# Performance work log

Hardware: AMD Instinct MI355X
Metric: run time of the kernel (lower is better)

The kernel has to match this reference:

```python
import jax, jax.numpy as jnp
import numpy as np

B, D_IMG, H, VOCAB, T = 16384, 2048, 512, 200, 20

def setup_inputs() -> dict:
    key = jax.random.key(0)
    ks = jax.random.split(key, 24)
    def w(k, shape, scale=0.05):
        return jax.random.normal(k, shape, dtype=jnp.float32) * scale
    return {
        "images": jax.random.normal(ks[0], (B, D_IMG), dtype=jnp.float32),
        "actions": jax.random.randint(ks[1], (B, T), 0, VOCAB, dtype=jnp.int64),
        # encoder: Linear(2048,512) -> ReLU -> Linear(512,512)
        "enc_w1": w(ks[2], (H, D_IMG)), "enc_b1": jnp.zeros((H,), jnp.float32),
        "enc_w2": w(ks[3], (H, H)),     "enc_b2": jnp.zeros((H,), jnp.float32),
        # GRUCell(512,512): gate order r, z, n (PyTorch convention)
        "gru_wih": w(ks[4], (3 * H, H)), "gru_bih": jnp.zeros((3 * H,), jnp.float32),
        "gru_whh": w(ks[5], (3 * H, H)), "gru_bhh": jnp.zeros((3 * H,), jnp.float32),
        # actor: 512->64->64->vocab
        "act_w1": w(ks[6], (64, H)),   "act_b1": jnp.zeros((64,), jnp.float32),
        "act_w2": w(ks[7], (64, 64)),  "act_b2": jnp.zeros((64,), jnp.float32),
        "act_w3": w(ks[8], (VOCAB, 64), 0.01), "act_b3": jnp.zeros((VOCAB,), jnp.float32),
        # critic: 512->64->64->1
        "cri_w1": w(ks[9], (64, H)),   "cri_b1": jnp.zeros((64,), jnp.float32),
        "cri_w2": w(ks[10], (64, 64)), "cri_b2": jnp.zeros((64,), jnp.float32),
        "cri_w3": w(ks[11], (1, 64), 0.02), "cri_b3": jnp.zeros((1,), jnp.float32),
    }

def reference(images, actions, enc_w1, enc_b1, enc_w2, enc_b2,
              gru_wih, gru_bih, gru_whh, gru_bhh,
              act_w1, act_b1, act_w2, act_b2, act_w3, act_b3,
              cri_w1, cri_b1, cri_w2, cri_b2, cri_w3, cri_b3):
    # encoder
    x = jax.nn.relu(images @ enc_w1.T + enc_b1) @ enc_w2.T + enc_b2  # [B, H]
    # input-side GRU gates are constant across steps (same x every step)
    xg = x @ gru_wih.T + gru_bih                                     # [B, 3H]
    xr, xz, xn = jnp.split(xg, 3, axis=-1)

    def step(hx, a_t):
        hg = hx @ gru_whh.T + gru_bhh
        hr, hz, hn = jnp.split(hg, 3, axis=-1)
        r = jax.nn.sigmoid(xr + hr)
        z = jax.nn.sigmoid(xz + hz)
        n = jnp.tanh(xn + r * hn)
        hx = (1.0 - z) * n + z * hx                                   # [B, H]
        # actor head -> categorical stats
        a_h = jnp.tanh(jnp.tanh(hx @ act_w1.T + act_b1) @ act_w2.T + act_b2)
        logits = a_h @ act_w3.T + act_b3                              # [B, V]
        logp = jax.nn.log_softmax(logits, axis=-1)
        lp = jnp.take_along_axis(logp, a_t[:, None], axis=1)[:, 0]    # [B]
        ent = -jnp.sum(jnp.exp(logp) * logp, axis=-1)                 # [B]
        # critic head
        c_h = jnp.tanh(jnp.tanh(hx @ cri_w1.T + cri_b1) @ cri_w2.T + cri_b2)
        v = c_h @ cri_w3.T + cri_b3                                   # [B, 1]
        return hx, (lp, ent, v)

    hx0 = jnp.zeros_like(x)
    _, (lps, ents, vs) = jax.lax.scan(step, hx0, actions.T)           # [T, B, ...]
    logprobs = lps.T                                                  # [B, T]
    entropies = ents.T                                                # [B, T]
    values = jnp.transpose(vs, (1, 0, 2))                             # [B, T, 1]
    return actions, logprobs, entropies, values
```

## Files before the change

### kernel.cpp

```cpp
#include <hip/hip_runtime.h>
#include <hip/hip_fp16.h>
#include <cstddef>
#include <cstdint>

#define BB 16384
#define DIMG 2048
#define HH 512
#define VOCAB 200
#define TT 20

using frag16 = __attribute__((ext_vector_type(8))) short;
using f32x4v = __attribute__((ext_vector_type(4))) float;

#define MFMA16(a, b, c) __builtin_amdgcn_mfma_f32_16x16x32_bf16((a), (b), (c), 0, 0, 0)

__device__ __forceinline__ float bf2f(unsigned short u) {
    union { unsigned int i; float f; } c; c.i = ((unsigned int)u) << 16; return c.f;
}
__device__ __forceinline__ unsigned short f2bf(float f) {
    union { float f; unsigned int i; } c; c.f = f;
    unsigned int u = c.i;
    u = (u + 0x7FFFu + ((u >> 16) & 1u)) >> 16;
    return (unsigned short)u;
}
__device__ __forceinline__ float sigf(float x) { return 1.f / (1.f + __expf(-x)); }
__device__ __forceinline__ float ftanh(float x) {
    return 1.f - 2.f / (1.f + __expf(2.f * x));
}
__device__ __forceinline__ void gload16(const void* g, void* l) {
    __builtin_amdgcn_global_load_lds(
        (__attribute__((address_space(1))) void*)g,
        (__attribute__((address_space(3))) void*)l, 16, 0, 0);
}


template<int ACT, int OM>
__global__ __launch_bounds__(256) void gemm_bt_mfma(
    const unsigned short* __restrict__ A, const unsigned short* __restrict__ W,
    const float* __restrict__ bias, void* __restrict__ Cv, int M, int N, int K)
{
    __shared__ unsigned short As[128 * 32];
    __shared__ unsigned short Ws[128 * 32];
    const int t = threadIdx.x;
    const int lane = t & 63, w = t >> 6;
    const int bm = blockIdx.x, bn = blockIdx.y;
    const int wm = (w >> 1) * 64, wn = (w & 1) * 64;

    f32x4v acc[4][4];
    #pragma unroll
    for (int i = 0; i < 4; ++i)
        #pragma unroll
        for (int j = 0; j < 4; ++j)
            #pragma unroll
            for (int r = 0; r < 4; ++r) acc[i][j][r] = 0.f;

    const unsigned short* Ag  = A + (size_t)(bm * 128 + (t >> 2)) * K + (t & 3) * 8;
    const unsigned short* Ag2 = A + (size_t)(bm * 128 + 64 + (t >> 2)) * K + (t & 3) * 8;
    const unsigned short* Wg  = W + (size_t)(bn * 128 + (t >> 2)) * K + (t & 3) * 8;
    const unsigned short* Wg2 = W + (size_t)(bn * 128 + 64 + (t >> 2)) * K + (t & 3) * 8;
    char* AsB = (char*)As; char* WsB = (char*)Ws;

    const int kIters = K >> 5;
    for (int ki = 0; ki < kIters; ++ki) {
        const int k0 = ki * 32;
        gload16(Ag  + k0, AsB + w * 1024);
        gload16(Ag2 + k0, AsB + 4096 + w * 1024);
        gload16(Wg  + k0, WsB + w * 1024);
        gload16(Wg2 + k0, WsB + 4096 + w * 1024);
        __syncthreads();
        frag16 af[4], bf[4];
        #pragma unroll
        for (int i = 0; i < 4; ++i) {
            af[i] = *(const frag16*)(AsB + (wm + i * 16 + (lane & 15)) * 64 + (lane >> 4) * 16);
            bf[i] = *(const frag16*)(WsB + (wn + i * 16 + (lane & 15)) * 64 + (lane >> 4) * 16);
        }
        #pragma unroll
        for (int i = 0; i < 4; ++i)
            #pragma unroll
            for (int j = 0; j < 4; ++j)
                acc[i][j] = MFMA16(af[i], bf[j], acc[i][j]);
        __syncthreads();
    }

    #pragma unroll
    for (int j = 0; j < 4; ++j) {
        const int gn = bn * 128 + wn + j * 16 + (lane & 15);
        const float bv = bias[gn];
        #pragma unroll
        for (int i = 0; i < 4; ++i) {
            #pragma unroll
            for (int r = 0; r < 4; ++r) {
                const size_t gm = (size_t)(bm * 128 + wm + i * 16 + (lane >> 4) * 4 + r);
                float v = acc[i][j][r] + bv;
                if (ACT == 1) v = fmaxf(v, 0.f);
                if (OM == 0)      ((float*)Cv)[gm * N + gn] = v;
                else if (OM == 1) ((unsigned short*)Cv)[gm * N + gn] = f2bf(v);
                else              ((__half*)Cv)[gm * N + gn] = __float2half(v);
            }
        }
    }
}

__device__ __forceinline__ void gru_body(
    unsigned short* lds,
    const unsigned short* __restrict__ hb, unsigned short* __restrict__ hob,
    const unsigned short* __restrict__ whhb, const float* __restrict__ bhh,
    const __half* __restrict__ xg, int bm, int bn, int t)
{
    char* L  = (char*)lds;
    char* LW = L + 16384;
    const int lane = t & 63, w = t >> 6;
    const int q = lane >> 4, m = lane & 15;
    const int qs = q ^ ((m >> 1) & 3);
    const int scol = ((t & 3) ^ ((t >> 3) & 3)) * 8;

    f32x4v acc[2][3][4];
    #pragma unroll
    for (int i = 0; i < 2; ++i)
        #pragma unroll
        for (int g = 0; g < 3; ++g)
            #pragma unroll
            for (int j = 0; j < 4; ++j)
                #pragma unroll
                for (int r = 0; r < 4; ++r) acc[i][g][j][r] = 0.f;

    const unsigned short* Ag  = hb + (size_t)(bm * 128 + (t >> 2)) * HH + scol;
    const unsigned short* Wg0 = whhb + (size_t)(0 * HH + bn * 64 + (t >> 2)) * HH + scol;
    const unsigned short* Wg1 = whhb + (size_t)(1 * HH + bn * 64 + (t >> 2)) * HH + scol;
    const unsigned short* Wg2 = whhb + (size_t)(2 * HH + bn * 64 + (t >> 2)) * HH + scol;

    for (int ki = 0; ki < 8; ++ki) {
        const int k0 = ki * 64;
        gload16(Ag + k0,                          L + w * 1024);
        gload16(Ag + k0 + 32,                     L + 8192 + w * 1024);
        gload16(Ag + (size_t)64 * HH + k0,        L + 4096 + w * 1024);
        gload16(Ag + (size_t)64 * HH + k0 + 32,   L + 8192 + 4096 + w * 1024);
        gload16(Wg0 + k0,      LW + w * 1024);
        gload16(Wg0 + k0 + 32, LW + 12288 + w * 1024);
        gload16(Wg1 + k0,      LW + 4096 + w * 1024);
        gload16(Wg1 + k0 + 32, LW + 12288 + 4096 + w * 1024);
        gload16(Wg2 + k0,      LW + 8192 + w * 1024);
        gload16(Wg2 + k0 + 32, LW + 12288 + 8192 + w * 1024);
        __syncthreads();
        #pragma unroll
        for (int kk = 0; kk < 2; ++kk) {
            frag16 af0 = *(const frag16*)(L + kk * 8192 +        (w * 16 + m) * 64 + qs * 16);
            frag16 af1 = *(const frag16*)(L + kk * 8192 + 4096 + (w * 16 + m) * 64 + qs * 16);
            #pragma unroll
            for (int g = 0; g < 3; ++g)
                #pragma unroll
                for (int j = 0; j < 4; ++j) {
                    frag16 bf = *(const frag16*)(LW + kk * 12288 + g * 4096 + (j * 16 + m) * 64 + qs * 16);
                    acc[0][g][j] = MFMA16(af0, bf, acc[0][g][j]);
                    acc[1][g][j] = MFMA16(af1, bf, acc[1][g][j]);
                }
        }
        __syncthreads();
    }

    float br[4], bz[4], bnn[4];
    #pragma unroll
    for (int j = 0; j < 4; ++j) {
        const int gc = bn * 64 + j * 16 + m;
        br[j] = bhh[gc]; bz[j] = bhh[HH + gc]; bnn[j] = bhh[2 * HH + gc];
    }

    #pragma unroll
    for (int half = 0; half < 2; ++half) {
        const int rbase = bm * 128 + half * 64;
        const __half* Xg = xg + (size_t)(rbase + (t >> 3)) * (3 * HH) + bn * 64 + (t & 7) * 8;
        #pragma unroll
        for (int c = 0; c < 6; ++c) {
            const int g = c >> 1, rh = c & 1;
            gload16(Xg + (size_t)rh * 32 * (3 * HH) + g * HH, L + g * 8192 + rh * 4096 + w * 1024);
        }
        const unsigned short* Hg = hb + (size_t)(rbase + (t >> 3)) * HH + bn * 64 + (t & 7) * 8;
        gload16(Hg,                   L + 24576 + w * 1024);
        gload16(Hg + (size_t)32 * HH, L + 24576 + 4096 + w * 1024);
        __syncthreads();

        unsigned short hv[4][4];
        #pragma unroll
        for (int r = 0; r < 4; ++r) {
            const int row = w * 16 + q * 4 + r;
            #pragma unroll
            for (int j = 0; j < 4; ++j) {
                const int col2 = (j * 16 + m) * 2;
                const float xr = __half2float(*(const __half*)(L + row * 128 + col2));
                const float xz = __half2float(*(const __half*)(L + 8192 + row * 128 + col2));
                const float xn = __half2float(*(const __half*)(L + 16384 + row * 128 + col2));
                const float ho = bf2f(*(const unsigned short*)(L + 24576 + row * 128 + col2));
                const float rg = sigf(xr + acc[half][0][j][r] + br[j]);
                const float zg = sigf(xz + acc[half][1][j][r] + bz[j]);
                const float ng = ftanh(xn + rg * (acc[half][2][j][r] + bnn[j]));
                hv[r][j] = f2bf((1.f - zg) * ng + zg * ho);
            }
        }
        __syncthreads();
        #pragma unroll
        for (int r = 0; r < 4; ++r) {
            const int row = w * 16 + q * 4 + r;
            #pragma unroll
            for (int j = 0; j < 4; ++j)
                *(unsigned short*)(L + 24576 + row * 128 + (j * 16 + m) * 2) = hv[r][j];
        }
        __syncthreads();
        {
            const int sr = t >> 2, sc = (t & 3) * 16;
            uint4 v0 = *(const uint4*)(L + 24576 + sr * 128 + sc * 2);
            uint4 v1 = *(const uint4*)(L + 24576 + sr * 128 + sc * 2 + 16);
            unsigned short* dst = hob + (size_t)(rbase + sr) * HH + bn * 64 + sc;
            *(uint4*)dst = v0;
            *(uint4*)(dst + 8) = v1;
        }
        __syncthreads();
    }
}

__device__ __forceinline__ void heads_body(
    unsigned short* lds, const unsigned short* __restrict__ hxb,
    const unsigned short* __restrict__ w1c, const unsigned short* __restrict__ w2s,
    const unsigned short* __restrict__ w3s,
    const float* __restrict__ b1c, const float* __restrict__ b2c,
    const float* __restrict__ b3s,
    const float* __restrict__ cw3, const float* __restrict__ cb3,
    const int* __restrict__ actions,
    float* __restrict__ out_lp, float* __restrict__ out_ent,
    float* __restrict__ out_v, int tstep, int hblk, int t)
{
    char* sH = (char*)lds;
    char* sW = (char*)lds + 4096;
    unsigned short* u1 = lds;
    const int lane = t & 63, w = t >> 6;
    const int q = lane >> 4, m = lane & 15;
    const int qs = q ^ ((m >> 1) & 3);
    const int scol = ((t & 3) ^ ((t >> 3) & 3)) * 8;
    const int row0 = hblk * 32;
    const int ri = (w & 1) * 16, ch = (w >> 1) * 64;

    f32x4v acc[4];
    #pragma unroll
    for (int j = 0; j < 4; ++j)
        #pragma unroll
        for (int r = 0; r < 4; ++r) acc[j][r] = 0.f;

    const unsigned short* Hrow = hxb + (size_t)(row0 + ((t >> 2) & 31)) * HH
                                 + (t >> 7) * 32 + scol;
    const unsigned short* Wrow[4]; int WldsOff[4];
    #pragma unroll
    for (int c = 0; c < 4; ++c) {
        const int kk = c & 1, rb = (c >> 1) * 64;
        Wrow[c] = w1c + (size_t)(rb + (t >> 2)) * HH + kk * 32 + scol;
        WldsOff[c] = kk * 8192 + rb * 64;
    }

    for (int ki = 0; ki < 8; ++ki) {
        const int k0 = ki * 64;
        gload16(Hrow + k0, sH + w * 1024);
        #pragma unroll
        for (int c = 0; c < 4; ++c)
            gload16(Wrow[c] + k0, sW + WldsOff[c] + w * 1024);
        __syncthreads();
        #pragma unroll
        for (int kk = 0; kk < 2; ++kk) {
            frag16 af = *(const frag16*)(sH + kk * 2048 + (ri + m) * 64 + qs * 16);
            #pragma unroll
            for (int j = 0; j < 4; ++j) {
                frag16 bf = *(const frag16*)(sW + kk * 8192 + (ch + j * 16 + m) * 64 + qs * 16);
                acc[j] = MFMA16(af, bf, acc[j]);
            }
        }
        __syncthreads();
    }
    #pragma unroll
    for (int j = 0; j < 4; ++j) {
        const int col = ch + j * 16 + m;
        const float bv = b1c[col];
        #pragma unroll
        for (int r = 0; r < 4; ++r)
            u1[(ri + q * 4 + r) * 136 + col] = f2bf(ftanh(acc[j][r] + bv));
    }
    __syncthreads();

    f32x4v acc2[4];
    #pragma unroll
    for (int j = 0; j < 4; ++j)
        #pragma unroll
        for (int r = 0; r < 4; ++r) acc2[j][r] = 0.f;
    #pragma unroll
    for (int kk = 0; kk < 2; ++kk) {
        frag16 af2 = *(const frag16*)(u1 + (ri + m) * 136 + ch + kk * 32 + q * 8);
        #pragma unroll
        for (int j = 0; j < 4; ++j) {
            frag16 bf2 = *(const frag16*)(w2s + (size_t)(ch + j * 16 + m) * 64 + kk * 32 + q * 8);
            acc2[j] = MFMA16(af2, bf2, acc2[j]);
        }
    }
    __syncthreads();
    #pragma unroll
    for (int j = 0; j < 4; ++j) {
        const int col = ch + j * 16 + m;
        const float bv = b2c[col];
        #pragma unroll
        for (int r = 0; r < 4; ++r)
            u1[(ri + q * 4 + r) * 136 + col] = f2bf(ftanh(acc2[j][r] + bv));
    }
    __syncthreads();

    if (w < 2) {
        f32x4v acc3[13];
        #pragma unroll
        for (int j = 0; j < 13; ++j)
            #pragma unroll
            for (int r = 0; r < 4; ++r) acc3[j][r] = 0.f;
        #pragma unroll
        for (int kk = 0; kk < 2; ++kk) {
            frag16 af3 = *(const frag16*)(u1 + (w * 16 + m) * 136 + kk * 32 + q * 8);
            #pragma unroll
            for (int j = 0; j < 13; ++j) {
                frag16 bf3 = *(const frag16*)(w3s + (size_t)(j * 16 + m) * 64 + kk * 32 + q * 8);
                acc3[j] = MFMA16(af3, bf3, acc3[j]);
            }
        }
        float bcol[13];
        #pragma unroll
        for (int j = 0; j < 13; ++j) bcol[j] = b3s[j * 16 + m];
        const bool vlast = (m < 8);
        #pragma unroll
        for (int r = 0; r < 4; ++r) {
            const int gr = row0 + w * 16 + 4 * q + r;
            const int a = actions[(size_t)gr * TT + tstep];
            float lg[13], mx = -1e30f;
            #pragma unroll
            for (int j = 0; j < 13; ++j) {
                float v = acc3[j][r] + bcol[j];
                lg[j] = (j < 12 || vlast) ? v : -1e30f;
                mx = fmaxf(mx, lg[j]);
            }
            #pragma unroll
            for (int o = 1; o < 16; o <<= 1) mx = fmaxf(mx, __shfl_xor(mx, o));
            float s1 = 0.f, s2 = 0.f, sel = 0.f;
            #pragma unroll
            for (int j = 0; j < 13; ++j) {
                float e = __expf(lg[j] - mx);
                s1 += e; s2 += e * lg[j];
                sel += (j * 16 + m == a) ? lg[j] : 0.f;
            }
            #pragma unroll
            for (int o = 1; o < 16; o <<= 1) {
                s1 += __shfl_xor(s1, o); s2 += __shfl_xor(s2, o); sel += __shfl_xor(sel, o);
            }
            const float lse = mx + __logf(s1);
            if (m == 0) {
                out_lp[(size_t)gr * TT + tstep]  = sel - lse;
                out_ent[(size_t)gr * TT + tstep] = lse - s2 / s1;
            }
        }
    } else {
        const int row = (w - 2) * 16 + m;
        const unsigned short* u2row = u1 + row * 136 + 64 + q * 16;
        float pv = 0.f;
        #pragma unroll
        for (int kk = 0; kk < 16; ++kk)
            pv += bf2f(u2row[kk]) * cw3[q * 16 + kk];
        pv += __shfl_xor(pv, 16);
        pv += __shfl_xor(pv, 32);
        if (q == 0) out_v[(size_t)(row0 + row) * TT + tstep] = pv + cb3[0];
    }
}

__global__ __launch_bounds__(256, 3) void step_fused(
    const unsigned short* __restrict__ hin, unsigned short* __restrict__ hout,
    const unsigned short* __restrict__ whhb, const float* __restrict__ bhh,
    const __half* __restrict__ xg,
    const unsigned short* __restrict__ w1c, const unsigned short* __restrict__ w2s,
    const unsigned short* __restrict__ w3s,
    const float* __restrict__ b1c, const float* __restrict__ b2c,
    const float* __restrict__ b3s,
    const float* __restrict__ cw3, const float* __restrict__ cb3,
    const int* __restrict__ actions,
    float* __restrict__ out_lp, float* __restrict__ out_ent,
    float* __restrict__ out_v, int hstep)
{
    __shared__ unsigned short lds[20480];
    const int b = blockIdx.x;
    if (b < 1024) {
        const int bm = ((b >> 6) << 3) | (b & 7);
        const int bn = (b >> 3) & 7;
        gru_body(lds, hin, hout, whhb, bhh, xg, bm, bn, threadIdx.x);
    } else if (hstep >= 0) {
        heads_body(lds, hin, w1c, w2s, w3s, b1c, b2c, b3s, cw3, cb3,
                   actions, out_lp, out_ent, out_v, hstep, b - 1024, threadIdx.x);
    }
}

__global__ __launch_bounds__(256) void heads_tail(
    const unsigned short* __restrict__ hx,
    const unsigned short* __restrict__ w1c, const unsigned short* __restrict__ w2s,
    const unsigned short* __restrict__ w3s,
    const float* __restrict__ b1c, const float* __restrict__ b2c,
    const float* __restrict__ b3s,
    const float* __restrict__ cw3, const float* __restrict__ cb3,
    const int* __restrict__ actions,
    float* __restrict__ out_lp, float* __restrict__ out_ent,
    float* __restrict__ out_v, int tstep)
{
    __shared__ unsigned short lds[10240];
    heads_body(lds, hx, w1c, w2s, w3s, b1c, b2c, b3s, cw3, cb3,
               actions, out_lp, out_ent, out_v, tstep, blockIdx.x, threadIdx.x);
}

__global__ void prep_heads(
    const float* __restrict__ aw1, const float* __restrict__ cw1,
    const float* __restrict__ aw2, const float* __restrict__ cw2,
    const float* __restrict__ aw3,
    const float* __restrict__ ab1, const float* __restrict__ cb1,
    const float* __restrict__ ab2, const float* __restrict__ cb2,
    const float* __restrict__ ab3,
    unsigned short* __restrict__ w1c, unsigned short* __restrict__ w2s,
    unsigned short* __restrict__ w3s,
    float* __restrict__ b1c, float* __restrict__ b2c, float* __restrict__ b3s)
{
    int i = blockIdx.x * 256 + threadIdx.x;
    if (i < 65536) { int r = i >> 9, c = i & 511;
        w1c[i] = f2bf(r < 64 ? aw1[r * 512 + c] : cw1[(r - 64) * 512 + c]); return; }
    i -= 65536;
    if (i < 8192) { int r = i >> 6, c = i & 63;
        w2s[i] = f2bf(r < 64 ? aw2[r * 64 + c] : cw2[(r - 64) * 64 + c]); return; }
    i -= 8192;
    if (i < 13312) { int r = i >> 6, c = i & 63;
        w3s[i] = f2bf(r < 200 ? aw3[r * 64 + c] : 0.f); return; }
    i -= 13312;
    if (i < 128) { b1c[i] = i < 64 ? ab1[i] : cb1[i - 64]; return; }
    i -= 128;
    if (i < 128) { b2c[i] = i < 64 ? ab2[i] : cb2[i - 64]; return; }
    i -= 128;
    if (i < 208) { b3s[i] = i < 200 ? ab3[i] : 0.f; return; }
}

__global__ void f2b_kernel(const float* __restrict__ s, unsigned short* __restrict__ d, int n) {
    int i = (blockIdx.x * 256 + threadIdx.x) * 4;
    if (i < n) {
        float4 v = *(const float4*)(s + i);
        ushort4 o;
        o.x = f2bf(v.x); o.y = f2bf(v.y); o.z = f2bf(v.z); o.w = f2bf(v.w);
        *(ushort4*)(d + i) = o;
    }
}

__global__ void copy_actions(const int* __restrict__ a, float* __restrict__ o, int n) {
    int i = blockIdx.x * 256 + threadIdx.x;
    if (i < n) o[i] = (float)a[i];
}

extern "C" void kernel_launch(void* const* d_in, const int* in_sizes, int n_in,
                              void* d_out, int out_size, void* d_ws, size_t ws_size,
                              hipStream_t stream)
{
    const float* images = (const float*)d_in[0];
    const int*   actions = (const int*)d_in[1];
    const float* enc_w1 = (const float*)d_in[2];
    const float* enc_b1 = (const float*)d_in[3];
    const float* enc_w2 = (const float*)d_in[4];
    const float* enc_b2 = (const float*)d_in[5];
    const float* gru_wih = (const float*)d_in[6];
    const float* gru_bih = (const float*)d_in[7];
    const float* gru_whh = (const float*)d_in[8];
    const float* gru_bhh = (const float*)d_in[9];
    const float* act_w1 = (const float*)d_in[10];
    const float* act_b1 = (const float*)d_in[11];
    const float* act_w2 = (const float*)d_in[12];
    const float* act_b2 = (const float*)d_in[13];
    const float* act_w3 = (const float*)d_in[14];
    const float* act_b3 = (const float*)d_in[15];
    const float* cri_w1 = (const float*)d_in[16];
    const float* cri_b1 = (const float*)d_in[17];
    const float* cri_w2 = (const float*)d_in[18];
    const float* cri_b2 = (const float*)d_in[19];
    const float* cri_w3 = (const float*)d_in[20];
    const float* cri_b3 = (const float*)d_in[21];

    char* ws = (char*)d_ws;
    unsigned short* imgb = (unsigned short*)ws;
    __half*         xg   = (__half*)ws;
    unsigned short* hbA  = (unsigned short*)(ws + 67108864);
    unsigned short* hbB  = (unsigned short*)(ws + 83886080);
    unsigned short* w1b  = (unsigned short*)(ws + 100663296);
    unsigned short* w2b  = (unsigned short*)(ws + 102760448);
    unsigned short* wihb = (unsigned short*)(ws + 103284736);
    unsigned short* whhb = (unsigned short*)(ws + 104857600);
    unsigned short* w1c  = (unsigned short*)(ws + 106430464);
    unsigned short* w2s  = (unsigned short*)(ws + 106561536);
    unsigned short* w3s  = (unsigned short*)(ws + 106577920);
    float*          b1c  = (float*)(ws + 106604544);
    float*          b2c  = (float*)(ws + 106605056);
    float*          b3s  = (float*)(ws + 106605568);

    float* out_act = (float*)d_out;
    float* out_lp  = out_act + (size_t)BB * TT;
    float* out_ent = out_lp  + (size_t)BB * TT;
    float* out_v   = out_ent + (size_t)BB * TT;

    dim3 blk(256);

    f2b_kernel<<<(BB * DIMG / 4 + 255) / 256, blk, 0, stream>>>(images, imgb, BB * DIMG);
    f2b_kernel<<<(512 * DIMG / 4 + 255) / 256, blk, 0, stream>>>(enc_w1, w1b, 512 * DIMG);
    f2b_kernel<<<(512 * 512 / 4 + 255) / 256, blk, 0, stream>>>(enc_w2, w2b, 512 * 512);
    f2b_kernel<<<(3 * HH * HH / 4 + 255) / 256, blk, 0, stream>>>(gru_wih, wihb, 3 * HH * HH);
    f2b_kernel<<<(3 * HH * HH / 4 + 255) / 256, blk, 0, stream>>>(gru_whh, whhb, 3 * HH * HH);
    prep_heads<<<(87504 + 255) / 256, blk, 0, stream>>>(
        act_w1, cri_w1, act_w2, cri_w2, act_w3,
        act_b1, cri_b1, act_b2, cri_b2, act_b3,
        w1c, w2s, w3s, b1c, b2c, b3s);

    gemm_bt_mfma<1, 1><<<dim3(BB / 128, 4), blk, 0, stream>>>(imgb, w1b, enc_b1, hbA, BB, 512, DIMG);
    gemm_bt_mfma<0, 1><<<dim3(BB / 128, 4), blk, 0, stream>>>(hbA, w2b, enc_b2, hbB, BB, 512, HH);
    gemm_bt_mfma<0, 2><<<dim3(BB / 128, 12), blk, 0, stream>>>(hbB, wihb, gru_bih, xg, BB, 1536, HH);

    hipMemsetAsync(hbA, 0, (size_t)BB * HH * 2, stream);
    copy_actions<<<(BB * TT + 255) / 256, blk, 0, stream>>>(actions, out_act, BB * TT);

    for (int t = 0; t < TT; ++t) {
        const unsigned short* hin = (t & 1) ? hbB : hbA;
        unsigned short*      hout = (t & 1) ? hbA : hbB;
        step_fused<<<1536, blk, 0, stream>>>(hin, hout, whhb, gru_bhh, xg,
            w1c, w2s, w3s, b1c, b2c, b3s, cri_w3, cri_b3, actions,
            out_lp, out_ent, out_v, t - 1);
    }
    heads_tail<<<512, blk, 0, stream>>>((TT & 1) ? hbB : hbA, w1c, w2s, w3s,
        b1c, b2c, b3s, cri_w3, cri_b3, actions, out_lp, out_ent, out_v, TT - 1);
}
```

Baseline: 1.417 ms.

## Double-buffer GRU weight tiles in LDS and load hidden-state fragments directly to registers

Restructures the GRU recurrent GEMM main loop into a two-stage software pipeline. W_hh tiles go into alternating LDS buffers with manual vmcnt waits and raw barriers, and the next stage is prefetched while the current one computes. The A operand (hidden state) now loads straight from global memory into register fragments instead of passing through LDS. LDS grows to 48KB per block and register pressure rises from the double-buffered A fragments, which may hurt occupancy under the 3-blocks launch bound.

```diff
diff --git a/kernel.cpp b/kernel.cpp
--- a/kernel.cpp
+++ b/kernel.cpp
@@ -107,8 +107,7 @@
     const unsigned short* __restrict__ whhb, const float* __restrict__ bhh,
     const __half* __restrict__ xg, int bm, int bn, int t)
 {
-    char* L  = (char*)lds;
-    char* LW = L + 16384;
+    char* L = (char*)lds;
     const int lane = t & 63, w = t >> 6;
     const int q = lane >> 4, m = lane & 15;
     const int qs = q ^ ((m >> 1) & 3);
@@ -124,39 +123,56 @@
                 #pragma unroll
                 for (int r = 0; r < 4; ++r) acc[i][g][j][r] = 0.f;
 
-    const unsigned short* Ag  = hb + (size_t)(bm * 128 + (t >> 2)) * HH + scol;
+    const unsigned short* A0 = hb + (size_t)(bm * 128 + w * 16 + m) * HH + q * 8;
+    const unsigned short* A1 = A0 + (size_t)64 * HH;
+
     const unsigned short* Wg0 = whhb + (size_t)(0 * HH + bn * 64 + (t >> 2)) * HH + scol;
     const unsigned short* Wg1 = whhb + (size_t)(1 * HH + bn * 64 + (t >> 2)) * HH + scol;
     const unsigned short* Wg2 = whhb + (size_t)(2 * HH + bn * 64 + (t >> 2)) * HH + scol;
 
+    frag16 aA[2][2][2];
+
+#define GRU_STAGE(B, K0) do {                                   \
+        char* Lb_ = L + (B) * 24576;                            \
+        gload16(Wg0 + (K0),      Lb_ + w * 1024);               \
+        gload16(Wg0 + (K0) + 32, Lb_ + 12288 + w * 1024);       \
+        gload16(Wg1 + (K0),      Lb_ + 4096 + w * 1024);        \
+        gload16(Wg1 + (K0) + 32, Lb_ + 12288 + 4096 + w * 1024);\
+        gload16(Wg2 + (K0),      Lb_ + 8192 + w * 1024);        \
+        gload16(Wg2 + (K0) + 32, Lb_ + 12288 + 8192 + w * 1024);\
+    } while (0)
+#define GRU_LOADA(S, K0) do {                                   \
+        aA[S][0][0] = *(const frag16*)(A0 + (K0));              \
+        aA[S][0][1] = *(const frag16*)(A0 + (K0) + 32);         \
+        aA[S][1][0] = *(const frag16*)(A1 + (K0));              \
+        aA[S][1][1] = *(const frag16*)(A1 + (K0) + 32);         \
+    } while (0)
+
+    GRU_STAGE(0, 0);   GRU_LOADA(0, 0);
+    GRU_STAGE(1, 64);  GRU_LOADA(1, 64);
+
+    #pragma unroll
     for (int ki = 0; ki < 8; ++ki) {
-        const int k0 = ki * 64;
-        gload16(Ag + k0,                          L + w * 1024);
-        gload16(Ag + k0 + 32,                     L + 8192 + w * 1024);
-        gload16(Ag + (size_t)64 * HH + k0,        L + 4096 + w * 1024);
-        gload16(Ag + (size_t)64 * HH + k0 + 32,   L + 8192 + 4096 + w * 1024);
-        gload16(Wg0 + k0,      LW + w * 1024);
-        gload16(Wg0 + k0 + 32, LW + 12288 + w * 1024);
-        gload16(Wg1 + k0,      LW + 4096 + w * 1024);
-        gload16(Wg1 + k0 + 32, LW + 12288 + 4096 + w * 1024);
-        gload16(Wg2 + k0,      LW + 8192 + w * 1024);
-        gload16(Wg2 + k0 + 32, LW + 12288 + 8192 + w * 1024);
-        __syncthreads();
+        if (ki == 7) asm volatile("s_waitcnt vmcnt(0)" ::: "memory");
+        else         asm volatile("s_waitcnt vmcnt(10)" ::: "memory");
+        __builtin_amdgcn_s_barrier();
+        char* Lb = L + (ki & 1) * 24576;
         #pragma unroll
         for (int kk = 0; kk < 2; ++kk) {
-            frag16 af0 = *(const frag16*)(L + kk * 8192 +        (w * 16 + m) * 64 + qs * 16);
-            frag16 af1 = *(const frag16*)(L + kk * 8192 + 4096 + (w * 16 + m) * 64 + qs * 16);
             #pragma unroll
             for (int g = 0; g < 3; ++g)
                 #pragma unroll
                 for (int j = 0; j < 4; ++j) {
-                    frag16 bf = *(const frag16*)(LW + kk * 12288 + g * 4096 + (j * 16 + m) * 64 + qs * 16);
-                    acc[0][g][j] = MFMA16(af0, bf, acc[0][g][j]);
-                    acc[1][g][j] = MFMA16(af1, bf, acc[1][g][j]);
+                    frag16 bf = *(const frag16*)(Lb + kk * 12288 + g * 4096 + (j * 16 + m) * 64 + qs * 16);
+                    acc[0][g][j] = MFMA16(aA[ki & 1][0][kk], bf, acc[0][g][j]);
+                    acc[1][g][j] = MFMA16(aA[ki & 1][1][kk], bf, acc[1][g][j]);
                 }
         }
-        __syncthreads();
-    }
+        __builtin_amdgcn_s_barrier();
+        if (ki < 6) { GRU_STAGE(ki & 1, (ki + 2) * 64); GRU_LOADA(ki & 1, (ki + 2) * 64); }
+    }
+#undef GRU_STAGE
+#undef GRU_LOADA
 
     float br[4], bz[4], bnn[4];
     #pragma unroll
@@ -382,7 +398,7 @@
     float* __restrict__ out_lp, float* __restrict__ out_ent,
     float* __restrict__ out_v, int hstep)
 {
-    __shared__ unsigned short lds[20480];
+    __shared__ unsigned short lds[24576];
     const int b = blockIdx.x;
     if (b < 1024) {
         const int bm = ((b >> 6) << 3) | (b & 7);
```

Result: no change. 1.424 ms (+0.4%).
